# Kernel tuning notes

Hardware: AMD Instinct MI355X
Metric: run time of the kernel (lower is better)

## Reference

```python
import jax, jax.numpy as jnp
import numpy as np

D_MODEL = 256
NCODES = 32


def setup_inputs() -> dict:
    key = jax.random.key(0)
    k1, k2 = jax.random.split(key)
    B, L = 64, 2048
    rev_repr = jax.random.normal(k1, (B, L, D_MODEL), dtype=jnp.float32)
    # xavier_normal for Linear(256 -> ncodes): std = sqrt(2/(fan_in+fan_out))
    std = (2.0 / (D_MODEL + NCODES)) ** 0.5
    W_codes = jax.random.normal(k2, (NCODES, D_MODEL), dtype=jnp.float32) * std
    return {"rev_repr": rev_repr, "W_codes": W_codes}


def reference(rev_repr, W_codes):
    # scores: (B, L, ncodes) = rev_repr @ W_codes.T
    scores = jnp.einsum('bld,kd->blk', rev_repr, W_codes)
    # softmax over the L (sequence) dimension, dim=1
    wts = jax.nn.softmax(scores, axis=1)
    # fused weighted-sum pooling: (B, ncodes, 256) — avoids (B,L,ncodes,256) intermediate
    contexts = jnp.einsum('blk,bld->bkd', wts, rev_repr)
    return contexts
```

## Files before the change

### kernel.cpp

```cpp
#include <hip/hip_runtime.h>
#include <math.h>

#define BATCH 64
#define LSEQ 2048
#define DMOD 256
#define KC 32
#define LCHUNK 256
#define LS 32
#define NSUB 8
#define PITCH_D 264
#define PITCH_L 40

typedef __bf16 bf16x8 __attribute__((ext_vector_type(8)));
typedef __bf16 bf16x4 __attribute__((ext_vector_type(4)));
typedef float f32x4 __attribute__((ext_vector_type(4)));

__global__ __launch_bounds__(256, 2) void fused_pool_kernel(
    const float* __restrict__ rev, const float* __restrict__ W,
    float* __restrict__ cPartial, float* __restrict__ zPartial) {
  __shared__ __align__(16) __bf16 sW[KC * PITCH_D];
  __shared__ __align__(16) __bf16 sRev[LS * PITCH_D];
  __shared__ __align__(16) __bf16 sRevT[DMOD * PITCH_L];
  __shared__ __align__(16) __bf16 sP[KC * PITCH_L];
  __shared__ float sZw[2][KC];

  const int tid = threadIdx.x;
  const int b = blockIdx.y;
  const int lc = blockIdx.x;
  const int lbase = lc * LCHUNK;
  const int lane = tid & 63;
  const int wave = tid >> 6;
  const int col = lane & 15;
  const int quad = lane >> 4;

  const int Mt = wave & 1;
  const int Nt = wave >> 1;

#pragma unroll
  for (int i = 0; i < 8; ++i) {
    int flat = tid + 256 * i;
    int kk = flat >> 6, c4 = flat & 63;
    float4 v = *(const float4*)(W + kk * DMOD + c4 * 4);
    bf16x4 h = {(__bf16)v.x, (__bf16)v.y, (__bf16)v.z, (__bf16)v.w};
    *(bf16x4*)(&sW[kk * PITCH_D + c4 * 4]) = h;
  }

  f32x4 acc2[8];
#pragma unroll
  for (int i = 0; i < 8; ++i) acc2[i] = (f32x4){0.f, 0.f, 0.f, 0.f};
  float zacc[4] = {0.f, 0.f, 0.f, 0.f};

  float4 pf[8];
#pragma unroll
  for (int i = 0; i < 8; ++i) {
    int slot = tid + 256 * i;
    int r = slot >> 6, c4 = slot & 63;
    pf[i] = *(const float4*)(rev + ((size_t)b * LSEQ + lbase + r) * DMOD + c4 * 4);
  }

  for (int sub = 0; sub < NSUB; ++sub) {
    __syncthreads();

#pragma unroll
    for (int i = 0; i < 8; ++i) {
      int slot = tid + 256 * i;
      int r = slot >> 6, c4 = slot & 63;
      float4 v = pf[i];
      bf16x4 h = {(__bf16)v.x, (__bf16)v.y, (__bf16)v.z, (__bf16)v.w};
      *(bf16x4*)(&sRev[r * PITCH_D + c4 * 4]) = h;
    }
    __syncthreads();

    if (sub + 1 < NSUB) {
      const int l1 = lbase + (sub + 1) * LS;
#pragma unroll
      for (int i = 0; i < 8; ++i) {
        int slot = tid + 256 * i;
        int r = slot >> 6, c4 = slot & 63;
        pf[i] = *(const float4*)(rev + ((size_t)b * LSEQ + l1 + r) * DMOD + c4 * 4);
      }
    }

#pragma unroll
    for (int j4 = 0; j4 < 4; ++j4) {
      bf16x8 v;
#pragma unroll
      for (int j = 0; j < 8; ++j) v[j] = sRev[(j4 * 8 + j) * PITCH_D + tid];
      *(bf16x8*)(&sRevT[tid * PITCH_L + j4 * 8]) = v;
    }

    f32x4 acc1 = {0.f, 0.f, 0.f, 0.f};
#pragma unroll
    for (int ks = 0; ks < 8; ++ks) {
      bf16x8 afrag = *(const bf16x8*)(&sW[(Mt * 16 + col) * PITCH_D + ks * 32 + quad * 8]);
      bf16x8 bfrag = *(const bf16x8*)(&sRev[(Nt * 16 + col) * PITCH_D + ks * 32 + quad * 8]);
      acc1 = __builtin_amdgcn_mfma_f32_16x16x32_bf16(afrag, bfrag, acc1, 0, 0, 0);
    }
#pragma unroll
    for (int reg = 0; reg < 4; ++reg) {
      float p = __expf(acc1[reg]);
      __bf16 ph = (__bf16)p;
      zacc[reg] += (float)ph;
      sP[(Mt * 16 + quad * 4 + reg) * PITCH_L + Nt * 16 + col] = ph;
    }
    __syncthreads();

    bf16x8 pa = *(const bf16x8*)(&sP[(Mt * 16 + col) * PITCH_L + quad * 8]);
#pragma unroll
    for (int nt = 0; nt < 8; ++nt) {
      int dt = Nt * 8 + nt;
      bf16x8 bb = *(const bf16x8*)(&sRevT[(dt * 16 + col) * PITCH_L + quad * 8]);
      acc2[nt] = __builtin_amdgcn_mfma_f32_16x16x32_bf16(pa, bb, acc2[nt], 0, 0, 0);
    }
  }

#pragma unroll
  for (int off = 1; off < 16; off <<= 1)
#pragma unroll
    for (int reg = 0; reg < 4; ++reg) zacc[reg] += __shfl_xor(zacc[reg], off, 64);
  if (col == 0) {
#pragma unroll
    for (int reg = 0; reg < 4; ++reg)
      sZw[Nt][Mt * 16 + quad * 4 + reg] = zacc[reg];
  }
  __syncthreads();
  if (tid < KC)
    zPartial[((size_t)b * 8 + lc) * KC + tid] = sZw[0][tid] + sZw[1][tid];

  float* dst = cPartial + (((size_t)b * 8 + lc) * KC) * DMOD;
#pragma unroll
  for (int nt = 0; nt < 8; ++nt) {
    int d = (Nt * 8 + nt) * 16 + col;
#pragma unroll
    for (int reg = 0; reg < 4; ++reg) {
      int k = Mt * 16 + quad * 4 + reg;
      dst[k * DMOD + d] = acc2[nt][reg];
    }
  }
}

__global__ __launch_bounds__(256) void reduce_kernel(
    const float* __restrict__ cPartial, const float* __restrict__ zPartial,
    float* __restrict__ out) {
  int idx = blockIdx.x * 256 + threadIdx.x;
  int b = idx >> 11;
  int k = (idx >> 6) & 31;
  float4 s = {0.f, 0.f, 0.f, 0.f};
  float z = 0.f;
#pragma unroll
  for (int lcc = 0; lcc < 8; ++lcc) {
    const float4 v = *(const float4*)(cPartial + ((((size_t)b * 8 + lcc) * KC + k) << 8) +
                                      ((idx & 63) << 2));
    s.x += v.x; s.y += v.y; s.z += v.z; s.w += v.w;
    z += zPartial[((size_t)b * 8 + lcc) * KC + k];
  }
  float zi = 1.0f / z;
  float4 o = {s.x * zi, s.y * zi, s.z * zi, s.w * zi};
  *(float4*)(out + ((size_t)idx << 2)) = o;
}

extern "C" void kernel_launch(void* const* d_in, const int* in_sizes, int n_in,
                              void* d_out, int out_size, void* d_ws,
                              size_t ws_size, hipStream_t stream) {
  const float* rev = (const float*)d_in[0];
  const float* W = (const float*)d_in[1];
  float* out = (float*)d_out;

  float* ws = (float*)d_ws;
  float* cPartial = ws;
  float* zPartial = cPartial + (size_t)BATCH * 8 * KC * DMOD;

  fused_pool_kernel<<<dim3(8, BATCH), dim3(256), 0, stream>>>(rev, W, cPartial,
                                                              zPartial);
  reduce_kernel<<<dim3(512), dim3(256), 0, stream>>>(cPartial, zPartial, out);
}
```

Before: 197.3 us.

## Halve L chunk, keep W fragments in registers, drop prefetch for higher occupancy

Halves the per-block sequence chunk so twice as many blocks launch, and raises launch bounds to allow four blocks per CU. W is no longer staged in shared memory; each wave holds its bf16 W fragments in registers and the first MFMA is transposed (rev as A, W as B). The register prefetch of the next rev tile is removed, and the LDS pitches are tightened with split 4-wide accesses to cut LDS footprint and bank conflicts. The cost is twice as many partial results for the reduce kernel to write and read, and no explicit overlap of global loads with compute.

```diff
diff --git a/kernel.cpp b/kernel.cpp
--- a/kernel.cpp
+++ b/kernel.cpp
@@ -5,24 +5,27 @@
 #define LSEQ 2048
 #define DMOD 256
 #define KC 32
-#define LCHUNK 256
+#define LCHUNK 128
 #define LS 32
-#define NSUB 8
+#define NSUB 4
 #define PITCH_D 264
-#define PITCH_L 40
+#define PITCH_T 36
 
 typedef __bf16 bf16x8 __attribute__((ext_vector_type(8)));
 typedef __bf16 bf16x4 __attribute__((ext_vector_type(4)));
 typedef float f32x4 __attribute__((ext_vector_type(4)));
 
-__global__ __launch_bounds__(256, 2) void fused_pool_kernel(
+static __device__ __forceinline__ bf16x8 cat8(bf16x4 a, bf16x4 b) {
+  return __builtin_shufflevector(a, b, 0, 1, 2, 3, 4, 5, 6, 7);
+}
+
+__global__ __launch_bounds__(256, 4) void fused_pool_kernel(
     const float* __restrict__ rev, const float* __restrict__ W,
     float* __restrict__ cPartial, float* __restrict__ zPartial) {
-  __shared__ __align__(16) __bf16 sW[KC * PITCH_D];
   __shared__ __align__(16) __bf16 sRev[LS * PITCH_D];
-  __shared__ __align__(16) __bf16 sRevT[DMOD * PITCH_L];
-  __shared__ __align__(16) __bf16 sP[KC * PITCH_L];
-  __shared__ float sZw[2][KC];
+  __shared__ __align__(16) __bf16 sRevT[DMOD * PITCH_T];
+  __shared__ __align__(16) __bf16 sP[KC * PITCH_T];
+  __shared__ float sZw[4][16];
 
   const int tid = threadIdx.x;
   const int b = blockIdx.y;
@@ -36,98 +39,86 @@
   const int Mt = wave & 1;
   const int Nt = wave >> 1;
 
+  bf16x8 wfrag[8];
+  {
+    const float* wrow = W + (Nt * 16 + col) * DMOD + quad * 8;
 #pragma unroll
-  for (int i = 0; i < 8; ++i) {
-    int flat = tid + 256 * i;
-    int kk = flat >> 6, c4 = flat & 63;
-    float4 v = *(const float4*)(W + kk * DMOD + c4 * 4);
-    bf16x4 h = {(__bf16)v.x, (__bf16)v.y, (__bf16)v.z, (__bf16)v.w};
-    *(bf16x4*)(&sW[kk * PITCH_D + c4 * 4]) = h;
+    for (int ks = 0; ks < 8; ++ks) {
+      float4 a = *(const float4*)(wrow + ks * 32);
+      float4 c = *(const float4*)(wrow + ks * 32 + 4);
+      bf16x4 lo = {(__bf16)a.x, (__bf16)a.y, (__bf16)a.z, (__bf16)a.w};
+      bf16x4 hi = {(__bf16)c.x, (__bf16)c.y, (__bf16)c.z, (__bf16)c.w};
+      wfrag[ks] = cat8(lo, hi);
+    }
   }
 
   f32x4 acc2[8];
 #pragma unroll
   for (int i = 0; i < 8; ++i) acc2[i] = (f32x4){0.f, 0.f, 0.f, 0.f};
-  float zacc[4] = {0.f, 0.f, 0.f, 0.f};
-
-  float4 pf[8];
-#pragma unroll
-  for (int i = 0; i < 8; ++i) {
-    int slot = tid + 256 * i;
-    int r = slot >> 6, c4 = slot & 63;
-    pf[i] = *(const float4*)(rev + ((size_t)b * LSEQ + lbase + r) * DMOD + c4 * 4);
-  }
+  float zl = 0.f;
 
   for (int sub = 0; sub < NSUB; ++sub) {
+    const int l0 = lbase + sub * LS;
     __syncthreads();
 
 #pragma unroll
     for (int i = 0; i < 8; ++i) {
       int slot = tid + 256 * i;
       int r = slot >> 6, c4 = slot & 63;
-      float4 v = pf[i];
+      float4 v = *(const float4*)(rev + ((size_t)b * LSEQ + l0 + r) * DMOD + c4 * 4);
       bf16x4 h = {(__bf16)v.x, (__bf16)v.y, (__bf16)v.z, (__bf16)v.w};
       *(bf16x4*)(&sRev[r * PITCH_D + c4 * 4]) = h;
     }
     __syncthreads();
 
-    if (sub + 1 < NSUB) {
-      const int l1 = lbase + (sub + 1) * LS;
-#pragma unroll
-      for (int i = 0; i < 8; ++i) {
-        int slot = tid + 256 * i;
-        int r = slot >> 6, c4 = slot & 63;
-        pf[i] = *(const float4*)(rev + ((size_t)b * LSEQ + l1 + r) * DMOD + c4 * 4);
-      }
-    }
-
 #pragma unroll
     for (int j4 = 0; j4 < 4; ++j4) {
-      bf16x8 v;
+      bf16x4 lo, hi;
 #pragma unroll
-      for (int j = 0; j < 8; ++j) v[j] = sRev[(j4 * 8 + j) * PITCH_D + tid];
-      *(bf16x8*)(&sRevT[tid * PITCH_L + j4 * 8]) = v;
+      for (int j = 0; j < 4; ++j) lo[j] = sRev[(j4 * 8 + j) * PITCH_D + tid];
+#pragma unroll
+      for (int j = 0; j < 4; ++j) hi[j] = sRev[(j4 * 8 + 4 + j) * PITCH_D + tid];
+      *(bf16x4*)(&sRevT[tid * PITCH_T + j4 * 8]) = lo;
+      *(bf16x4*)(&sRevT[tid * PITCH_T + j4 * 8 + 4]) = hi;
     }
 
     f32x4 acc1 = {0.f, 0.f, 0.f, 0.f};
 #pragma unroll
     for (int ks = 0; ks < 8; ++ks) {
-      bf16x8 afrag = *(const bf16x8*)(&sW[(Mt * 16 + col) * PITCH_D + ks * 32 + quad * 8]);
-      bf16x8 bfrag = *(const bf16x8*)(&sRev[(Nt * 16 + col) * PITCH_D + ks * 32 + quad * 8]);
-      acc1 = __builtin_amdgcn_mfma_f32_16x16x32_bf16(afrag, bfrag, acc1, 0, 0, 0);
+      bf16x8 af = *(const bf16x8*)(&sRev[(Mt * 16 + col) * PITCH_D + ks * 32 + quad * 8]);
+      acc1 = __builtin_amdgcn_mfma_f32_16x16x32_bf16(af, wfrag[ks], acc1, 0, 0, 0);
     }
 #pragma unroll
     for (int reg = 0; reg < 4; ++reg) {
       float p = __expf(acc1[reg]);
       __bf16 ph = (__bf16)p;
-      zacc[reg] += (float)ph;
-      sP[(Mt * 16 + quad * 4 + reg) * PITCH_L + Nt * 16 + col] = ph;
+      zl += (float)ph;
+      sP[(Nt * 16 + col) * PITCH_T + Mt * 16 + quad * 4 + reg] = ph;
     }
     __syncthreads();
 
-    bf16x8 pa = *(const bf16x8*)(&sP[(Mt * 16 + col) * PITCH_L + quad * 8]);
+    bf16x4 pa0 = *(const bf16x4*)(&sP[(Mt * 16 + col) * PITCH_T + quad * 8]);
+    bf16x4 pa1 = *(const bf16x4*)(&sP[(Mt * 16 + col) * PITCH_T + quad * 8 + 4]);
+    bf16x8 pa = cat8(pa0, pa1);
 #pragma unroll
     for (int nt = 0; nt < 8; ++nt) {
-      int dt = Nt * 8 + nt;
-      bf16x8 bb = *(const bf16x8*)(&sRevT[(dt * 16 + col) * PITCH_L + quad * 8]);
-      acc2[nt] = __builtin_amdgcn_mfma_f32_16x16x32_bf16(pa, bb, acc2[nt], 0, 0, 0);
+      int drow = (Nt * 8 + nt) * 16 + col;
+      bf16x4 b0 = *(const bf16x4*)(&sRevT[drow * PITCH_T + quad * 8]);
+      bf16x4 b1 = *(const bf16x4*)(&sRevT[drow * PITCH_T + quad * 8 + 4]);
+      acc2[nt] = __builtin_amdgcn_mfma_f32_16x16x32_bf16(pa, cat8(b0, b1), acc2[nt], 0, 0, 0);
     }
   }
 
-#pragma unroll
-  for (int off = 1; off < 16; off <<= 1)
-#pragma unroll
-    for (int reg = 0; reg < 4; ++reg) zacc[reg] += __shfl_xor(zacc[reg], off, 64);
-  if (col == 0) {
-#pragma unroll
-    for (int reg = 0; reg < 4; ++reg)
-      sZw[Nt][Mt * 16 + quad * 4 + reg] = zacc[reg];
+  zl += __shfl_xor(zl, 16, 64);
+  zl += __shfl_xor(zl, 32, 64);
+  if (quad == 0) sZw[wave][col] = zl;
+  __syncthreads();
+  if (tid < KC) {
+    int Ntt = tid >> 4, c = tid & 15;
+    zPartial[((size_t)b * 16 + lc) * KC + tid] = sZw[2 * Ntt][c] + sZw[2 * Ntt + 1][c];
   }
-  __syncthreads();
-  if (tid < KC)
-    zPartial[((size_t)b * 8 + lc) * KC + tid] = sZw[0][tid] + sZw[1][tid];
 
-  float* dst = cPartial + (((size_t)b * 8 + lc) * KC) * DMOD;
+  float* dst = cPartial + (((size_t)b * 16 + lc) * KC) * DMOD;
 #pragma unroll
   for (int nt = 0; nt < 8; ++nt) {
     int d = (Nt * 8 + nt) * 16 + col;
@@ -148,11 +139,12 @@
   float4 s = {0.f, 0.f, 0.f, 0.f};
   float z = 0.f;
 #pragma unroll
-  for (int lcc = 0; lcc < 8; ++lcc) {
-    const float4 v = *(const float4*)(cPartial + ((((size_t)b * 8 + lcc) * KC + k) << 8) +
+  for (int lcc = 0; lcc < 16; ++lcc) {
+    const float4 v = *(const float4*)(cPartial +
+                                      ((((size_t)b * 16 + lcc) * KC + k) << 8) +
                                       ((idx & 63) << 2));
     s.x += v.x; s.y += v.y; s.z += v.z; s.w += v.w;
-    z += zPartial[((size_t)b * 8 + lcc) * KC + k];
+    z += zPartial[((size_t)b * 16 + lcc) * KC + k];
   }
   float zi = 1.0f / z;
   float4 o = {s.x * zi, s.y * zi, s.z * zi, s.w * zi};
@@ -168,9 +160,9 @@
 
   float* ws = (float*)d_ws;
   float* cPartial = ws;
-  float* zPartial = cPartial + (size_t)BATCH * 8 * KC * DMOD;
+  float* zPartial = cPartial + (size_t)BATCH * 16 * KC * DMOD;
 
-  fused_pool_kernel<<<dim3(8, BATCH), dim3(256), 0, stream>>>(rev, W, cPartial,
-                                                              zPartial);
+  fused_pool_kernel<<<dim3(16, BATCH), dim3(256), 0, stream>>>(rev, W, cPartial,
+                                                               zPartial);
   reduce_kernel<<<dim3(512), dim3(256), 0, stream>>>(cPartial, zPartial, out);
 }
```

Result: slower. 206.3 us (+4.6%).
